# Kernel tuning notes

Measured on AMD Instinct MI355X. Metric: run time of the kernel, lower is better.

Reference implementation:

```python
import jax, jax.numpy as jnp
import numpy as np

N_NODES = 100_000
N_EDGES = 1_600_000
D_IN = 64
D_OUT = 64


def setup_inputs() -> dict:
    key = jax.random.key(0)
    k1, k2, k3, k4, k5, k6, k7, k8 = jax.random.split(key, 8)
    edge_row = jax.random.randint(k1, (N_EDGES,), 0, N_NODES, dtype=jnp.int32)
    edge_col = jax.random.randint(k2, (N_EDGES,), 0, N_NODES, dtype=jnp.int32)
    # normalized adjacency values (e.g. sym-normalized weights)
    edge_vals = jax.random.uniform(k3, (N_EDGES,), dtype=jnp.float32)
    node_feat = jax.random.normal(k4, (N_NODES, D_IN), dtype=jnp.float32)
    scale = (6.0 / (D_IN + D_OUT)) ** 0.5  # xavier_uniform
    W1 = jax.random.uniform(k5, (D_IN, D_OUT), minval=-scale, maxval=scale, dtype=jnp.float32)
    W2 = jax.random.uniform(k6, (D_IN, D_OUT), minval=-scale, maxval=scale, dtype=jnp.float32)
    b1 = jax.random.normal(k7, (D_OUT,), dtype=jnp.float32) * 0.02
    b2 = jax.random.normal(k8, (D_OUT,), dtype=jnp.float32) * 0.02
    return {"edge_row": edge_row, "edge_col": edge_col, "edge_vals": edge_vals,
            "node_feat": node_feat, "W1": W1, "b1": b1, "W2": W2, "b2": b2}


def reference(edge_row, edge_col, edge_vals, node_feat, W1, b1, W2, b2):
    # agg = sparse.mm(mat, node_feat): gather neighbor feats, weight, scatter-add
    gathered = edge_vals[:, None] * node_feat[edge_col]          # [E, D_IN]
    agg_feat = jax.ops.segment_sum(gathered, edge_row, num_segments=N_NODES)  # [N, D_IN]
    leaky = lambda x: jnp.where(x >= 0, x, 0.2 * x)
    part1 = leaky(agg_feat @ W1 + b1)                            # [N, D_OUT]
    part2 = leaky((agg_feat * node_feat) @ W2 + b2)              # [N, D_OUT]
    # dropout is identity in eval mode
    return part1 + part2
```

## Files before the change

kernel.cpp:

```cpp
#include <hip/hip_runtime.h>

#define NN 100000
#define NE 1600000
#define D 64
#define NB 256
#define EPB (NE / NB)
#define BROWS 128
#define HROWS 64
#define NBK ((NN + BROWS - 1) / BROWS)
#define NH (NBK * NB)
#define SCAN_BLK 1024
#define NSB ((NH + SCAN_BLK - 1) / SCAN_BLK)
#define CAP 1536
#define REG_E 12
#define WT_LD 72

static constexpr size_t OFF_AGG16  = 0;
static constexpr size_t OFF_BH     = 12800000;
static constexpr size_t OFF_BS     = 13600768;
static constexpr size_t OFF_COARSE = 13601792;
static constexpr size_t OFF_F16    = 26401792;

typedef short bf16x8 __attribute__((ext_vector_type(8)));
typedef float f32x4 __attribute__((ext_vector_type(4)));

__device__ __forceinline__ unsigned short f32_to_bf16_rn(float x) {
    unsigned int u = __float_as_uint(x);
    u += 0x7FFFu + ((u >> 16) & 1u);
    return (unsigned short)(u >> 16);
}
__device__ __forceinline__ float bf16_to_f32(unsigned int lo16) {
    return __uint_as_float(lo16 << 16);
}

__global__ __launch_bounds__(256) void conv_k(const float* __restrict__ feat,
                                              unsigned short* __restrict__ feat16) {
    int i = blockIdx.x * blockDim.x + threadIdx.x;
    if (i >= NN * D / 8) return;
    const float4 f0 = *reinterpret_cast<const float4*>(&feat[i * 8]);
    const float4 f1 = *reinterpret_cast<const float4*>(&feat[i * 8 + 4]);
    uint4 o;
    o.x = f32_to_bf16_rn(f0.x) | ((unsigned int)f32_to_bf16_rn(f0.y) << 16);
    o.y = f32_to_bf16_rn(f0.z) | ((unsigned int)f32_to_bf16_rn(f0.w) << 16);
    o.z = f32_to_bf16_rn(f1.x) | ((unsigned int)f32_to_bf16_rn(f1.y) << 16);
    o.w = f32_to_bf16_rn(f1.z) | ((unsigned int)f32_to_bf16_rn(f1.w) << 16);
    *reinterpret_cast<uint4*>(&feat16[i * 8]) = o;
}

__global__ __launch_bounds__(256) void bhist_k(const int* __restrict__ rows,
                                               int* __restrict__ bh) {
    __shared__ int h[NBK];
    for (int i = threadIdx.x; i < NBK; i += 256) h[i] = 0;
    __syncthreads();
    const int e0 = blockIdx.x * EPB;
    for (int e = e0 + threadIdx.x; e < e0 + EPB; e += 256)
        atomicAdd(&h[rows[e] >> 7], 1);
    __syncthreads();
    for (int i = threadIdx.x; i < NBK; i += 256) bh[i * NB + blockIdx.x] = h[i];
}

__global__ __launch_bounds__(256) void scan1_k(int* __restrict__ a,
                                               int* __restrict__ bsum) {
    __shared__ int tsum[256];
    const int base = blockIdx.x * SCAN_BLK + threadIdx.x * 4;
    int v[4];
    int s = 0;
#pragma unroll
    for (int i = 0; i < 4; ++i) {
        int idx = base + i;
        v[i] = (idx < NH) ? a[idx] : 0;
        s += v[i];
    }
    tsum[threadIdx.x] = s;
    __syncthreads();
    int x = s;
    for (int off = 1; off < 256; off <<= 1) {
        int y = (threadIdx.x >= off) ? tsum[threadIdx.x - off] : 0;
        __syncthreads();
        x += y;
        tsum[threadIdx.x] = x;
        __syncthreads();
    }
    int run = x - s;
#pragma unroll
    for (int i = 0; i < 4; ++i) {
        int idx = base + i;
        if (idx < NH) a[idx] = run;
        run += v[i];
    }
    if (threadIdx.x == 255) bsum[blockIdx.x] = x;
}

__global__ void scan2_k(int* __restrict__ bsum) {
    __shared__ int s[256];
    int i = threadIdx.x;
    int v = (i < NSB) ? bsum[i] : 0;
    s[i] = v;
    __syncthreads();
    int x = v;
    for (int off = 1; off < 256; off <<= 1) {
        int y = (i >= off) ? s[i - off] : 0;
        __syncthreads();
        x += y;
        s[i] = x;
        __syncthreads();
    }
    if (i < NSB) bsum[i] = x - v;
}

__global__ __launch_bounds__(256) void bin_k(const int* __restrict__ rows,
                                             const int* __restrict__ cols,
                                             const float* __restrict__ vals,
                                             const int* __restrict__ bh,
                                             const int* __restrict__ bsum,
                                             int2* __restrict__ coarse) {
    __shared__ int cur[NBK];
    for (int i = threadIdx.x; i < NBK; i += 256) {
        int idx = i * NB + blockIdx.x;
        cur[i] = bh[idx] + bsum[idx >> 10];
    }
    __syncthreads();
    const int e0 = blockIdx.x * EPB;
    for (int e = e0 + threadIdx.x; e < e0 + EPB; e += 256) {
        int r = rows[e];
        int b = r >> 7;
        int p = atomicAdd(&cur[b], 1);
        coarse[p] = make_int2(((r & 127) << 17) | cols[e], __float_as_int(vals[e]));
    }
}

__global__ __launch_bounds__(256) void bgather_k(const int* __restrict__ bh,
                                                 const int* __restrict__ bsum,
                                                 const int2* __restrict__ coarse,
                                                 const unsigned short* __restrict__ feat16,
                                                 unsigned short* __restrict__ agg16) {
    __shared__ int2 se[CAP];
    __shared__ int hist[HROWS];
    __shared__ int rsl[HROWS];
    const int blk = blockIdx.x;
    const int b = blk >> 1;
    const int h = blk & 1;
    const int i0 = b * NB;
    const int i1 = (b + 1) * NB;
    const int start = bh[i0] + bsum[i0 >> 10];
    int end = (b == NBK - 1) ? NE : (bh[i1] + bsum[i1 >> 10]);
    if (end - start > 2 * CAP) end = start + 2 * CAP;

    const int tid = threadIdx.x;

    int2 ev[REG_E];
#pragma unroll
    for (int j = 0; j < REG_E; ++j) {
        int i = start + tid + j * 256;
        ev[j] = (i < end) ? coarse[i] : make_int2(-1, 0);
    }

    if (tid < HROWS) hist[tid] = 0;
    __syncthreads();
#pragma unroll
    for (int j = 0; j < REG_E; ++j) {
        int rl = ((unsigned)ev[j].x) >> 17;
        if ((rl >> 6) == h) atomicAdd(&hist[rl & 63], 1);
    }
    __syncthreads();
    if (tid < HROWS) rsl[tid] = hist[tid];
    __syncthreads();
    for (int off = 1; off < HROWS; off <<= 1) {
        int y = 0;
        if (tid < HROWS && tid >= off) y = rsl[tid - off];
        __syncthreads();
        if (tid < HROWS) rsl[tid] += y;
        __syncthreads();
    }
    if (tid < HROWS) hist[tid] = rsl[tid] - hist[tid];
    __syncthreads();
#pragma unroll
    for (int j = 0; j < REG_E; ++j) {
        int rl = ((unsigned)ev[j].x) >> 17;
        if ((rl >> 6) == h) {
            int p = atomicAdd(&hist[rl & 63], 1);
            if (p < CAP) se[p] = ev[j];
        }
    }
    __syncthreads();

    const int lane = tid & 63;
    const int wv = tid >> 6;
    const int g = lane >> 3;
    const int t = lane & 7;
    const int rowbase = b * BROWS + h * HROWS;

    for (int rl = wv * 16; rl < wv * 16 + 16; ++rl) {
        int r0 = (rl == 0) ? 0 : rsl[rl - 1];
        int r1 = rsl[rl];
        if (r0 > CAP) r0 = CAP;
        if (r1 > CAP) r1 = CAP;
        float acc[8];
#pragma unroll
        for (int k = 0; k < 8; ++k) acc[k] = 0.f;
        for (int base2 = r0; base2 < r1; base2 += 64) {
            int nn = r1 - base2;
            if (nn > 64) nn = 64;
            int c = 0;
            float v = 0.f;
            if (lane < nn) {
                int2 e2 = se[base2 + lane];
                c = e2.x & 0x1FFFF;
                v = __int_as_float(e2.y);
            }
            const int niter = (nn + 7) >> 3;
            for (int jj = 0; jj < niter; ++jj) {
                int src = (jj << 3) + g;
                int cj = __shfl(c, src);
                float vj = __shfl(v, src);
                const uint4 f =
                    *reinterpret_cast<const uint4*>(&feat16[(size_t)cj * D + (t << 3)]);
                acc[0] += vj * bf16_to_f32(f.x & 0xffffu);
                acc[1] += vj * bf16_to_f32(f.x >> 16);
                acc[2] += vj * bf16_to_f32(f.y & 0xffffu);
                acc[3] += vj * bf16_to_f32(f.y >> 16);
                acc[4] += vj * bf16_to_f32(f.z & 0xffffu);
                acc[5] += vj * bf16_to_f32(f.z >> 16);
                acc[6] += vj * bf16_to_f32(f.w & 0xffffu);
                acc[7] += vj * bf16_to_f32(f.w >> 16);
            }
        }
#pragma unroll
        for (int off = 8; off <= 32; off <<= 1) {
#pragma unroll
            for (int k = 0; k < 8; ++k) acc[k] += __shfl_xor(acc[k], off);
        }
        const int r = rowbase + rl;
        if (lane < 8 && r < NN) {
            uint4 o;
            o.x = f32_to_bf16_rn(acc[0]) | ((unsigned int)f32_to_bf16_rn(acc[1]) << 16);
            o.y = f32_to_bf16_rn(acc[2]) | ((unsigned int)f32_to_bf16_rn(acc[3]) << 16);
            o.z = f32_to_bf16_rn(acc[4]) | ((unsigned int)f32_to_bf16_rn(acc[5]) << 16);
            o.w = f32_to_bf16_rn(acc[6]) | ((unsigned int)f32_to_bf16_rn(acc[7]) << 16);
            *reinterpret_cast<uint4*>(&agg16[(size_t)r * D + (t << 3)]) = o;
        }
    }
}

__global__ __launch_bounds__(256) void mlp_k(const unsigned short* __restrict__ agg16,
                                             const unsigned short* __restrict__ feat16,
                                             const float* __restrict__ W1,
                                             const float* __restrict__ b1,
                                             const float* __restrict__ W2,
                                             const float* __restrict__ b2,
                                             float* __restrict__ out) {
    __shared__ unsigned short W1t[64 * WT_LD];
    __shared__ unsigned short W2t[64 * WT_LD];
    for (int idx = threadIdx.x; idx < 4096; idx += 256) {
        int k = idx >> 6, n = idx & 63;
        W1t[n * WT_LD + k] = f32_to_bf16_rn(W1[idx]);
        W2t[n * WT_LD + k] = f32_to_bf16_rn(W2[idx]);
    }
    __syncthreads();

    const int lane = threadIdx.x & 63;
    const int wv = threadIdx.x >> 6;
    const int lm = lane & 15;
    const int lk = lane >> 4;
    const int rowA = blockIdx.x * 64 + wv * 16 + lm;
    const bool valid = rowA < NN;
    const size_t abase = (size_t)rowA * D;

    f32x4 acc1[4], acc2[4];
#pragma unroll
    for (int nb = 0; nb < 4; ++nb) {
        acc1[nb] = (f32x4){0.f, 0.f, 0.f, 0.f};
        acc2[nb] = (f32x4){0.f, 0.f, 0.f, 0.f};
    }

    union U { uint4 u; bf16x8 v; };

#pragma unroll
    for (int kk = 0; kk < 2; ++kk) {
        const int k0 = kk * 32 + lk * 8;
        U ua, uf, um;
        ua.u = make_uint4(0, 0, 0, 0);
        uf.u = make_uint4(0, 0, 0, 0);
        if (valid) {
            ua.u = *reinterpret_cast<const uint4*>(&agg16[abase + k0]);
            uf.u = *reinterpret_cast<const uint4*>(&feat16[abase + k0]);
        }
        {
            const unsigned int* au = &ua.u.x;
            const unsigned int* fu = &uf.u.x;
            unsigned int* mu = &um.u.x;
#pragma unroll
            for (int q = 0; q < 4; ++q) {
                float lo = bf16_to_f32(au[q] & 0xffffu) * bf16_to_f32(fu[q] & 0xffffu);
                float hi = bf16_to_f32(au[q] >> 16) * bf16_to_f32(fu[q] >> 16);
                mu[q] = f32_to_bf16_rn(lo) | ((unsigned int)f32_to_bf16_rn(hi) << 16);
            }
        }
#pragma unroll
        for (int nb = 0; nb < 4; ++nb) {
            U b1f, b2f;
            b1f.v = *reinterpret_cast<const bf16x8*>(&W1t[(nb * 16 + lm) * WT_LD + k0]);
            b2f.v = *reinterpret_cast<const bf16x8*>(&W2t[(nb * 16 + lm) * WT_LD + k0]);
            acc1[nb] = __builtin_amdgcn_mfma_f32_16x16x32_bf16(ua.v, b1f.v, acc1[nb], 0, 0, 0);
            acc2[nb] = __builtin_amdgcn_mfma_f32_16x16x32_bf16(um.v, b2f.v, acc2[nb], 0, 0, 0);
        }
    }

#pragma unroll
    for (int nb = 0; nb < 4; ++nb) {
        const int col = nb * 16 + lm;
        const float bb1 = b1[col];
        const float bb2 = b2[col];
#pragma unroll
        for (int j = 0; j < 4; ++j) {
            const int row = blockIdx.x * 64 + wv * 16 + lk * 4 + j;
            if (row < NN) {
                float x1 = acc1[nb][j] + bb1;
                float x2 = acc2[nb][j] + bb2;
                x1 = x1 >= 0.f ? x1 : 0.2f * x1;
                x2 = x2 >= 0.f ? x2 : 0.2f * x2;
                out[(size_t)row * D + col] = x1 + x2;
            }
        }
    }
}

extern "C" void kernel_launch(void* const* d_in, const int* in_sizes, int n_in,
                              void* d_out, int out_size, void* d_ws, size_t ws_size,
                              hipStream_t stream) {
    const int* rows = (const int*)d_in[0];
    const int* cols = (const int*)d_in[1];
    const float* vals = (const float*)d_in[2];
    const float* feat = (const float*)d_in[3];
    const float* W1 = (const float*)d_in[4];
    const float* b1 = (const float*)d_in[5];
    const float* W2 = (const float*)d_in[6];
    const float* b2 = (const float*)d_in[7];
    float* out = (float*)d_out;

    char* ws = (char*)d_ws;
    unsigned short* agg16 = (unsigned short*)(ws + OFF_AGG16);
    int* bh = (int*)(ws + OFF_BH);
    int* bsum = (int*)(ws + OFF_BS);
    int2* coarse = (int2*)(ws + OFF_COARSE);
    unsigned short* feat16 = (unsigned short*)(ws + OFF_F16);

    conv_k<<<(NN * D / 8 + 255) / 256, 256, 0, stream>>>(feat, feat16);

    bhist_k<<<NB, 256, 0, stream>>>(rows, bh);
    scan1_k<<<NSB, 256, 0, stream>>>(bh, bsum);
    scan2_k<<<1, 256, 0, stream>>>(bsum);
    bin_k<<<NB, 256, 0, stream>>>(rows, cols, vals, bh, bsum, coarse);

    bgather_k<<<NBK * 2, 256, 0, stream>>>(bh, bsum, coarse, feat16, agg16);

    const int ntiles = (NN + 63) / 64;
    mlp_k<<<ntiles, 256, 0, stream>>>(agg16, feat16, W1, b1, W2, b2, out);
}
```

Baseline: 115.9 us.

## Fuse MLP epilogue into gather kernel and pretranspose weights in conversion kernel

The dense two-matrix MLP is moved into the gather kernel. Each 64-row half-bucket writes its aggregated bf16 rows to shared memory and then runs the MFMA matmuls directly, so the agg16 global round trip and one kernel launch are removed. Weight transposition and bf16 conversion move into the feature conversion kernel, which writes the weights once to workspace, and the fused kernel reads them from global/L2 instead of LDS. In exchange the fused kernel uses more LDS and registers, which may lower occupancy, and the weight reads now go through the cache rather than shared memory.

```diff
diff --git a/kernel.cpp b/kernel.cpp
--- a/kernel.cpp
+++ b/kernel.cpp
@@ -13,9 +13,10 @@
 #define NSB ((NH + SCAN_BLK - 1) / SCAN_BLK)
 #define CAP 1536
 #define REG_E 12
-#define WT_LD 72
-
-static constexpr size_t OFF_AGG16  = 0;
+#define AT_LD 72
+
+static constexpr size_t OFF_WT1    = 0;
+static constexpr size_t OFF_WT2    = 8192;
 static constexpr size_t OFF_BH     = 12800000;
 static constexpr size_t OFF_BS     = 13600768;
 static constexpr size_t OFF_COARSE = 13601792;
@@ -34,17 +35,29 @@
 }
 
 __global__ __launch_bounds__(256) void conv_k(const float* __restrict__ feat,
-                                              unsigned short* __restrict__ feat16) {
+                                              unsigned short* __restrict__ feat16,
+                                              const float* __restrict__ W1,
+                                              const float* __restrict__ W2,
+                                              unsigned short* __restrict__ Wt1,
+                                              unsigned short* __restrict__ Wt2) {
     int i = blockIdx.x * blockDim.x + threadIdx.x;
-    if (i >= NN * D / 8) return;
-    const float4 f0 = *reinterpret_cast<const float4*>(&feat[i * 8]);
-    const float4 f1 = *reinterpret_cast<const float4*>(&feat[i * 8 + 4]);
-    uint4 o;
-    o.x = f32_to_bf16_rn(f0.x) | ((unsigned int)f32_to_bf16_rn(f0.y) << 16);
-    o.y = f32_to_bf16_rn(f0.z) | ((unsigned int)f32_to_bf16_rn(f0.w) << 16);
-    o.z = f32_to_bf16_rn(f1.x) | ((unsigned int)f32_to_bf16_rn(f1.y) << 16);
-    o.w = f32_to_bf16_rn(f1.z) | ((unsigned int)f32_to_bf16_rn(f1.w) << 16);
-    *reinterpret_cast<uint4*>(&feat16[i * 8]) = o;
+    if (i < NN * D / 8) {
+        const float4 f0 = *reinterpret_cast<const float4*>(&feat[i * 8]);
+        const float4 f1 = *reinterpret_cast<const float4*>(&feat[i * 8 + 4]);
+        uint4 o;
+        o.x = f32_to_bf16_rn(f0.x) | ((unsigned int)f32_to_bf16_rn(f0.y) << 16);
+        o.y = f32_to_bf16_rn(f0.z) | ((unsigned int)f32_to_bf16_rn(f0.w) << 16);
+        o.z = f32_to_bf16_rn(f1.x) | ((unsigned int)f32_to_bf16_rn(f1.y) << 16);
+        o.w = f32_to_bf16_rn(f1.z) | ((unsigned int)f32_to_bf16_rn(f1.w) << 16);
+        *reinterpret_cast<uint4*>(&feat16[i * 8]) = o;
+    } else {
+        int widx = i - NN * D / 8;
+        if (widx < 4096) {
+            int k = widx >> 6, n = widx & 63;
+            Wt1[n * 64 + k] = f32_to_bf16_rn(W1[widx]);
+            Wt2[n * 64 + k] = f32_to_bf16_rn(W2[widx]);
+        }
+    }
 }
 
 __global__ __launch_bounds__(256) void bhist_k(const int* __restrict__ rows,
@@ -133,10 +146,15 @@
                                                  const int* __restrict__ bsum,
                                                  const int2* __restrict__ coarse,
                                                  const unsigned short* __restrict__ feat16,
-                                                 unsigned short* __restrict__ agg16) {
+                                                 const unsigned short* __restrict__ Wt1,
+                                                 const unsigned short* __restrict__ Wt2,
+                                                 const float* __restrict__ b1,
+                                                 const float* __restrict__ b2,
+                                                 float* __restrict__ out) {
     __shared__ int2 se[CAP];
     __shared__ int hist[HROWS];
     __shared__ int rsl[HROWS];
+    __shared__ unsigned short at[HROWS * AT_LD];
     const int blk = blockIdx.x;
     const int b = blk >> 1;
     const int h = blk & 1;
@@ -230,41 +248,22 @@
 #pragma unroll
             for (int k = 0; k < 8; ++k) acc[k] += __shfl_xor(acc[k], off);
         }
-        const int r = rowbase + rl;
-        if (lane < 8 && r < NN) {
+        if (lane < 8) {
             uint4 o;
             o.x = f32_to_bf16_rn(acc[0]) | ((unsigned int)f32_to_bf16_rn(acc[1]) << 16);
             o.y = f32_to_bf16_rn(acc[2]) | ((unsigned int)f32_to_bf16_rn(acc[3]) << 16);
             o.z = f32_to_bf16_rn(acc[4]) | ((unsigned int)f32_to_bf16_rn(acc[5]) << 16);
             o.w = f32_to_bf16_rn(acc[6]) | ((unsigned int)f32_to_bf16_rn(acc[7]) << 16);
-            *reinterpret_cast<uint4*>(&agg16[(size_t)r * D + (t << 3)]) = o;
-        }
-    }
-}
-
-__global__ __launch_bounds__(256) void mlp_k(const unsigned short* __restrict__ agg16,
-                                             const unsigned short* __restrict__ feat16,
-                                             const float* __restrict__ W1,
-                                             const float* __restrict__ b1,
-                                             const float* __restrict__ W2,
-                                             const float* __restrict__ b2,
-                                             float* __restrict__ out) {
-    __shared__ unsigned short W1t[64 * WT_LD];
-    __shared__ unsigned short W2t[64 * WT_LD];
-    for (int idx = threadIdx.x; idx < 4096; idx += 256) {
-        int k = idx >> 6, n = idx & 63;
-        W1t[n * WT_LD + k] = f32_to_bf16_rn(W1[idx]);
-        W2t[n * WT_LD + k] = f32_to_bf16_rn(W2[idx]);
-    }
-    __syncthreads();
-
-    const int lane = threadIdx.x & 63;
-    const int wv = threadIdx.x >> 6;
+            *reinterpret_cast<uint4*>(&at[rl * AT_LD + (t << 3)]) = o;
+        }
+    }
+    __syncthreads();
+
     const int lm = lane & 15;
     const int lk = lane >> 4;
-    const int rowA = blockIdx.x * 64 + wv * 16 + lm;
+    const int rowA = rowbase + wv * 16 + lm;
     const bool valid = rowA < NN;
-    const size_t abase = (size_t)rowA * D;
+    const size_t fbase = (size_t)rowA * D;
 
     f32x4 acc1[4], acc2[4];
 #pragma unroll
@@ -279,12 +278,10 @@
     for (int kk = 0; kk < 2; ++kk) {
         const int k0 = kk * 32 + lk * 8;
         U ua, uf, um;
-        ua.u = make_uint4(0, 0, 0, 0);
+        ua.u = *reinterpret_cast<const uint4*>(&at[(wv * 16 + lm) * AT_LD + k0]);
         uf.u = make_uint4(0, 0, 0, 0);
-        if (valid) {
-            ua.u = *reinterpret_cast<const uint4*>(&agg16[abase + k0]);
-            uf.u = *reinterpret_cast<const uint4*>(&feat16[abase + k0]);
-        }
+        if (valid)
+            uf.u = *reinterpret_cast<const uint4*>(&feat16[fbase + k0]);
         {
             const unsigned int* au = &ua.u.x;
             const unsigned int* fu = &uf.u.x;
@@ -299,8 +296,8 @@
 #pragma unroll
         for (int nb = 0; nb < 4; ++nb) {
             U b1f, b2f;
-            b1f.v = *reinterpret_cast<const bf16x8*>(&W1t[(nb * 16 + lm) * WT_LD + k0]);
-            b2f.v = *reinterpret_cast<const bf16x8*>(&W2t[(nb * 16 + lm) * WT_LD + k0]);
+            b1f.u = *reinterpret_cast<const uint4*>(&Wt1[(nb * 16 + lm) * 64 + k0]);
+            b2f.u = *reinterpret_cast<const uint4*>(&Wt2[(nb * 16 + lm) * 64 + k0]);
             acc1[nb] = __builtin_amdgcn_mfma_f32_16x16x32_bf16(ua.v, b1f.v, acc1[nb], 0, 0, 0);
             acc2[nb] = __builtin_amdgcn_mfma_f32_16x16x32_bf16(um.v, b2f.v, acc2[nb], 0, 0, 0);
         }
@@ -313,7 +310,7 @@
         const float bb2 = b2[col];
 #pragma unroll
         for (int j = 0; j < 4; ++j) {
-            const int row = blockIdx.x * 64 + wv * 16 + lk * 4 + j;
+            const int row = rowbase + wv * 16 + lk * 4 + j;
             if (row < NN) {
                 float x1 = acc1[nb][j] + bb1;
                 float x2 = acc2[nb][j] + bb2;
@@ -339,21 +336,21 @@
     float* out = (float*)d_out;
 
     char* ws = (char*)d_ws;
-    unsigned short* agg16 = (unsigned short*)(ws + OFF_AGG16);
+    unsigned short* Wt1 = (unsigned short*)(ws + OFF_WT1);
+    unsigned short* Wt2 = (unsigned short*)(ws + OFF_WT2);
     int* bh = (int*)(ws + OFF_BH);
     int* bsum = (int*)(ws + OFF_BS);
     int2* coarse = (int2*)(ws + OFF_COARSE);
     unsigned short* feat16 = (unsigned short*)(ws + OFF_F16);
 
-    conv_k<<<(NN * D / 8 + 255) / 256, 256, 0, stream>>>(feat, feat16);
+    conv_k<<<(NN * D / 8 + 4096 + 255) / 256, 256, 0, stream>>>(
+        feat, feat16, W1, W2, Wt1, Wt2);
 
     bhist_k<<<NB, 256, 0, stream>>>(rows, bh);
     scan1_k<<<NSB, 256, 0, stream>>>(bh, bsum);
     scan2_k<<<1, 256, 0, stream>>>(bsum);
     bin_k<<<NB, 256, 0, stream>>>(rows, cols, vals, bh, bsum, coarse);
 
-    bgather_k<<<NBK * 2, 256, 0, stream>>>(bh, bsum, coarse, feat16, agg16);
-
-    const int ntiles = (NN + 63) / 64;
-    mlp_k<<<ntiles, 256, 0, stream>>>(agg16, feat16, W1, b1, W2, b2, out);
-}
+    bgather_k<<<NBK * 2, 256, 0, stream>>>(bh, bsum, coarse, feat16,
+                                           Wt1, Wt2, b1, b2, out);
+}
```

Measured after the change: 123.3 us. 1.06x slower.
